# Optimization experiments

Hardware: AMD Instinct MI355X
Metric: run time of the kernel (lower is better)

## Reference

```python
import jax, jax.numpy as jnp
import numpy as np

NUM_HEADS = 32
NUM_KV = 8
HEAD_DIM = 128


def rotate_half(x):
    half = x.shape[-1] // 2
    x1, x2 = x[..., :half], x[..., half:]
    return jnp.concatenate([-x2, x1], axis=-1)


def apply_rope(x, cos, sin):
    # x: [B, H, S, D]; cos/sin: [S, D] broadcast over batch and heads
    return x * cos + rotate_half(x) * sin


def setup_inputs() -> dict:
    key = jax.random.key(0)
    kx, kqkv, kout = jax.random.split(key, 3)
    B, S, H = 2, 2048, 4096
    x = jax.random.normal(kx, (B, S, H), dtype=jnp.float32)
    Wqkv = jax.random.normal(kqkv, (H, NUM_HEADS * HEAD_DIM + 2 * NUM_KV * HEAD_DIM), dtype=jnp.float32) * (H ** -0.5)
    Wout = jax.random.normal(kout, (H, H), dtype=jnp.float32) * (H ** -0.5)
    # realistic RoPE tables (seq, head_dim)
    inv_freq = 1.0 / (10000.0 ** (np.arange(0, HEAD_DIM, 2, dtype=np.float32) / HEAD_DIM))
    freqs = np.outer(np.arange(S, dtype=np.float32), inv_freq)  # [S, D/2]
    emb = np.concatenate([freqs, freqs], axis=-1)  # [S, D]
    cos = jnp.asarray(np.cos(emb), dtype=jnp.float32)
    sin = jnp.asarray(np.sin(emb), dtype=jnp.float32)
    return {"x": x, "cos": cos, "sin": sin, "Wqkv": Wqkv, "Wout": Wout}


def reference(x, cos, sin, Wqkv, Wout):
    B, S, H = x.shape
    nh, nkv, hd = NUM_HEADS, NUM_KV, HEAD_DIM
    qkv = x @ Wqkv  # [B, S, (nh+2*nkv)*hd]
    q, k, v = jnp.split(qkv, [nh * hd, nh * hd + nkv * hd], axis=-1)
    q = q.reshape(B, S, nh, hd).transpose(0, 2, 1, 3)   # [B, nh, S, hd]
    k = k.reshape(B, S, nkv, hd).transpose(0, 2, 1, 3)  # [B, nkv, S, hd]
    v = v.reshape(B, S, nkv, hd).transpose(0, 2, 1, 3)
    q = apply_rope(q, cos, sin)
    k = apply_rope(k, cos, sin)
    group = nh // nkv
    k = jnp.repeat(k, group, axis=1)  # repeat_interleave over head dim
    v = jnp.repeat(v, group, axis=1)
    scale = 1.0 / jnp.sqrt(jnp.asarray(hd, dtype=x.dtype))
    scores = jnp.einsum('bhqd,bhkd->bhqk', q, k) * scale  # [B, nh, S, S]
    causal = jnp.triu(jnp.ones((S, S), dtype=bool), k=1)
    scores = jnp.where(causal, -jnp.inf, scores)
    w = jax.nn.softmax(scores, axis=-1)
    out = jnp.einsum('bhqk,bhkd->bhqd', w, v)  # [B, nh, S, hd]
    out = out.transpose(0, 2, 1, 3).reshape(B, S, nh * hd)
    return out @ Wout
```

## Files before the change

kernel.cpp:

```cpp
#include <hip/hip_runtime.h>

typedef unsigned short u16;
typedef __attribute__((ext_vector_type(8))) short s16x8;
typedef __attribute__((ext_vector_type(4))) short s16x4;
typedef __attribute__((ext_vector_type(4))) float f32x4;

#define DEVI __device__ __forceinline__

DEVI u16 f2b(float f) {
  union { float f; unsigned u; } v; v.f = f;
  unsigned r = v.u + 0x7FFFu + ((v.u >> 16) & 1u);
  return (u16)(r >> 16);
}
DEVI float b2f(u16 h) {
  union { unsigned u; float f; } v; v.u = ((unsigned)h) << 16;
  return v.f;
}

typedef const __attribute__((address_space(1))) void gas_void;
typedef __attribute__((address_space(3))) void las_void;
DEVI void gload16(const void* g, void* l) {
  __builtin_amdgcn_global_load_lds((gas_void*)g, (las_void*)l, 16, 0, 0);
}

__global__ void conv_bf16(const float* __restrict__ in, u16* __restrict__ out, int n8) {
  int i = blockIdx.x * 256 + threadIdx.x;
  if (i >= n8) return;
  const float* p = in + (size_t)i * 8;
  float4 u = *(const float4*)p;
  float4 v = *(const float4*)(p + 4);
  s16x8 o = {(short)f2b(u.x), (short)f2b(u.y), (short)f2b(u.z), (short)f2b(u.w),
             (short)f2b(v.x), (short)f2b(v.y), (short)f2b(v.z), (short)f2b(v.w)};
  *(s16x8*)(out + (size_t)i * 8) = o;
}

__global__ void trans_bf16(const float* __restrict__ W, u16* __restrict__ Wt, int K, int N) {
  __shared__ __attribute__((aligned(16))) u16 tile[64][68];
  const int t = threadIdx.x;
  const int n0 = blockIdx.x * 64, k0 = blockIdx.y * 64;
#pragma unroll
  for (int i = 0; i < 4; ++i) {
    int c = i * 256 + t;
    int r = c >> 4, q = c & 15;
    float4 v = *(const float4*)(W + (size_t)(k0 + r) * N + n0 + q * 4);
    s16x4 o = {(short)f2b(v.x), (short)f2b(v.y), (short)f2b(v.z), (short)f2b(v.w)};
    *(s16x4*)&tile[r][q * 4] = o;
  }
  __syncthreads();
#pragma unroll
  for (int i = 0; i < 2; ++i) {
    int c = i * 256 + t;
    int n_ = c >> 3, ck = (c & 7) * 8;
    s16x8 o;
#pragma unroll
    for (int j = 0; j < 8; ++j) o[j] = (short)tile[ck + j][n_];
    *(s16x8*)(Wt + (size_t)(n0 + n_) * K + k0 + ck) = o;
  }
}

template <typename TC>
__global__ __launch_bounds__(512, 2) void gemm256(const u16* __restrict__ A,
                                                  const u16* __restrict__ Bt,
                                                  TC* __restrict__ C, int M, int N, int K) {
  __shared__ __attribute__((aligned(16))) u16 As[2][2][128 * 64];
  __shared__ __attribute__((aligned(16))) u16 Bs[2][2][128 * 64];
  const int t = threadIdx.x;
  const int nbn = N >> 8;
  const int nwg = (M >> 8) * nbn;
  const int chunk = nwg >> 3;
  const int id = (blockIdx.x & 7) * chunk + (blockIdx.x >> 3);
  const int row0 = (id / nbn) << 8, col0 = (id % nbn) << 8;
  const int w = t >> 6, lane = t & 63, lc = lane & 15, lg = lane >> 4;
  const int wqm = (w >> 2) * 64;
  const int wqn = (w & 3) * 32;
  const int sw7 = lc & 7;

  const f32x4 FZ = {0.f, 0.f, 0.f, 0.f};
  f32x4 acc[4][4][2];
#pragma unroll
  for (int q = 0; q < 4; ++q)
#pragma unroll
    for (int i = 0; i < 4; ++i)
#pragma unroll
      for (int j = 0; j < 2; ++j) acc[q][i][j] = FZ;

  const int s_r0 = t >> 3, s_r1 = (512 + t) >> 3;
  const int s_s = t & 7;

#define STG_A(kt, H, sl)                                                                   \
  {                                                                                        \
    gload16(A + (size_t)(row0 + (H)*128 + s_r0) * K + ((kt) << 6) + ((s_s ^ (s_r0 & 7)) << 3), \
            (u16*)As[sl][H] + t * 8);                                                      \
    gload16(A + (size_t)(row0 + (H)*128 + s_r1) * K + ((kt) << 6) + ((s_s ^ (s_r1 & 7)) << 3), \
            (u16*)As[sl][H] + (512 + t) * 8);                                              \
  }
#define STG_B(kt, H, sl)                                                                   \
  {                                                                                        \
    gload16(Bt + (size_t)(col0 + (H)*128 + s_r0) * K + ((kt) << 6) + ((s_s ^ (s_r0 & 7)) << 3), \
            (u16*)Bs[sl][H] + t * 8);                                                      \
    gload16(Bt + (size_t)(col0 + (H)*128 + s_r1) * K + ((kt) << 6) + ((s_s ^ (s_r1 & 7)) << 3), \
            (u16*)Bs[sl][H] + (512 + t) * 8);                                              \
  }
#define LOAD_A(MH, buf)                                                           \
  _Pragma("unroll") for (int mf = 0; mf < 4; ++mf)                                \
  _Pragma("unroll") for (int ks = 0; ks < 2; ++ks)                                \
    af[mf][ks] = *(const s16x8*)(As[buf][MH] + (wqm + mf * 16 + lc) * 64 +        \
                                 (((ks * 4 + lg) ^ sw7) << 3));
#define LOAD_B(NH, buf, DST)                                                      \
  _Pragma("unroll") for (int nf = 0; nf < 2; ++nf)                                \
  _Pragma("unroll") for (int ks = 0; ks < 2; ++ks)                                \
    DST[nf][ks] = *(const s16x8*)(Bs[buf][NH] + (wqn + nf * 16 + lc) * 64 +       \
                                  (((ks * 4 + lg) ^ sw7) << 3));
#define MFMA_Q(q, BV)                                                             \
  _Pragma("unroll") for (int ks = 0; ks < 2; ++ks)                                \
  _Pragma("unroll") for (int mf = 0; mf < 4; ++mf)                                \
  _Pragma("unroll") for (int nf = 0; nf < 2; ++nf)                                \
    acc[q][mf][nf] = __builtin_amdgcn_mfma_f32_16x16x32_bf16(                     \
        af[mf][ks], BV[nf][ks], acc[q][mf][nf], 0, 0, 0);
#define BAR __builtin_amdgcn_s_barrier()
#define PRIO1 __builtin_amdgcn_s_setprio(1)
#define PRIO0 __builtin_amdgcn_s_setprio(0)
#define WAIT4 asm volatile("s_waitcnt vmcnt(4)" ::: "memory")

  s16x8 af[4][2], bfv0[2][2], bfv1[2][2];
  const int NT = K >> 6, NI = NT >> 1, TM = NT - 1;

  STG_A(0, 0, 0) STG_B(0, 0, 0) STG_B(0, 1, 0) STG_A(0, 1, 0)
  STG_A(1, 0, 1) STG_B(1, 1, 1)
  WAIT4;
  BAR;

  for (int i = 0; i < NI; ++i) {
    const int t1 = 2 * i + 1;
    const int t2 = (2 * i + 2) & TM, t3 = (2 * i + 3) & TM;
    LOAD_A(0, 0) LOAD_B(0, 0, bfv0)
    STG_B(t1, 0, 1)
    BAR; PRIO1; MFMA_Q(0, bfv0) PRIO0; BAR;
    LOAD_B(1, 0, bfv1)
    STG_A(t1, 1, 1)
    BAR; PRIO1; MFMA_Q(1, bfv1) PRIO0; BAR;
    LOAD_A(1, 0)
    STG_A(t2, 0, 0)
    BAR; PRIO1; MFMA_Q(2, bfv1) PRIO0; BAR;
    STG_B(t2, 1, 0)
    BAR; PRIO1; MFMA_Q(3, bfv0) PRIO0;
    WAIT4;
    BAR;
    LOAD_A(0, 1) LOAD_B(0, 1, bfv0)
    STG_B(t2, 0, 0)
    BAR; PRIO1; MFMA_Q(0, bfv0) PRIO0; BAR;
    LOAD_B(1, 1, bfv1)
    STG_A(t2, 1, 0)
    BAR; PRIO1; MFMA_Q(1, bfv1) PRIO0; BAR;
    LOAD_A(1, 1)
    STG_A(t3, 0, 1)
    BAR; PRIO1; MFMA_Q(2, bfv1) PRIO0; BAR;
    STG_B(t3, 1, 1)
    BAR; PRIO1; MFMA_Q(3, bfv0) PRIO0;
    WAIT4;
    BAR;
  }
  asm volatile("s_waitcnt vmcnt(0)" ::: "memory");
  BAR;
#undef STG_A
#undef STG_B
#undef LOAD_A
#undef LOAD_B
#undef MFMA_Q
#undef BAR
#undef PRIO1
#undef PRIO0
#undef WAIT4

  const int qmh[4] = {0, 0, 1, 1}, qnh[4] = {0, 1, 1, 0};
#pragma unroll
  for (int q = 0; q < 4; ++q)
#pragma unroll
    for (int mf = 0; mf < 4; ++mf)
#pragma unroll
      for (int nf = 0; nf < 2; ++nf)
#pragma unroll
        for (int r = 0; r < 4; ++r) {
          const int rg = row0 + qmh[q] * 128 + wqm + mf * 16 + lg * 4 + r;
          const int cg = col0 + qnh[q] * 128 + wqn + nf * 16 + lc;
          if constexpr (sizeof(TC) == 2)
            ((u16*)C)[(size_t)rg * N + cg] = f2b(acc[q][mf][nf][r]);
          else
            ((float*)C)[(size_t)rg * N + cg] = acc[q][mf][nf][r];
        }
}

__global__ void rope_kernel(u16* __restrict__ qkv, const float* __restrict__ cosb,
                            const float* __restrict__ sinb) {
  const int bs = blockIdx.x;
  const int s = bs & 2047;
  u16* row = qkv + (size_t)bs * 6144;
  const float* cr = cosb + s * 128;
  const float* sr = sinb + s * 128;
  for (int p = threadIdx.x; p < 320; p += 256) {
    int head = p >> 3, dc = (p & 7) * 8;
    int ci = head * 128 + dc;
    s16x8 a = *(const s16x8*)&row[ci];
    s16x8 bb = *(const s16x8*)&row[ci + 64];
    float4 c0 = *(const float4*)(cr + dc), c1 = *(const float4*)(cr + dc + 4);
    float4 s0 = *(const float4*)(sr + dc), s1 = *(const float4*)(sr + dc + 4);
    float cv[8] = {c0.x, c0.y, c0.z, c0.w, c1.x, c1.y, c1.z, c1.w};
    float sv[8] = {s0.x, s0.y, s0.z, s0.w, s1.x, s1.y, s1.z, s1.w};
    s16x8 o1, o2;
#pragma unroll
    for (int j = 0; j < 8; ++j) {
      float x1 = b2f((u16)a[j]), x2 = b2f((u16)bb[j]);
      o1[j] = (short)f2b(x1 * cv[j] - x2 * sv[j]);
      o2[j] = (short)f2b(x2 * cv[j] + x1 * sv[j]);
    }
    *(s16x8*)&row[ci] = o1;
    *(s16x8*)&row[ci + 64] = o2;
  }
}

__global__ void vtrans_kernel(const u16* __restrict__ qkv, u16* __restrict__ v_t) {
  __shared__ __attribute__((aligned(16))) u16 tile[64][72];
  const int t = threadIdx.x;
  const int s0 = blockIdx.x * 64;
  const int d0 = blockIdx.y * 64;
  const int bk = blockIdx.z;
  const int b = bk >> 3, kvh = bk & 7;
  const int slot = t & 7, r0 = t >> 3;
#pragma unroll
  for (int i = 0; i < 2; ++i) {
    int s_ = r0 + 32 * i;
    *(s16x8*)&tile[s_][slot * 8] =
        *(const s16x8*)(qkv + (size_t)(b * 2048 + s0 + s_) * 6144 + 5120 + kvh * 128 + d0 + slot * 8);
  }
  __syncthreads();
#pragma unroll
  for (int i = 0; i < 2; ++i) {
    int d_ = r0 + 32 * i;
    s16x8 v;
#pragma unroll
    for (int j = 0; j < 8; ++j) v[j] = (short)tile[slot * 8 + j][d_];
    *(s16x8*)(v_t + ((size_t)bk * 128 + d0 + d_) * 2048 + s0 + slot * 8) = v;
  }
}

__global__ void __launch_bounds__(256, 2) attn_kernel(const u16* __restrict__ qkv,
                                                      const u16* __restrict__ v_t,
                                                      u16* __restrict__ attn) {
  __shared__ __attribute__((aligned(16))) u16 Ks[64][136];
  __shared__ __attribute__((aligned(16))) u16 Vs[128][72];
  __shared__ __attribute__((aligned(16))) u16 Ps[4][32][72];
  const int t = threadIdx.x;
  const int f = blockIdx.x;
  const int xcd = f & 7, ix = f >> 3;
  const int g = (xcd << 1) | (ix >> 6);
  const int r_ = ix & 63;
  const int b = g >> 3, kvh = g & 7;
  const int qt = 15 - (r_ >> 2);
  const int h = kvh * 4 + (r_ & 3);
  const int q0 = qt * 128;
  const int w = t >> 6, lane = t & 63, lc = lane & 15, lg = lane >> 4;
  const int qw = q0 + w * 32;

  const u16* qbase = qkv + (size_t)(b * 2048) * 6144 + h * 128;
  const u16* kbase = qkv + (size_t)(b * 2048) * 6144 + 4096 + kvh * 128;
  const u16* vbase = v_t + (size_t)(b * 8 + kvh) * 128 * 2048;

  s16x8 qf[2][4];
#pragma unroll
  for (int mf = 0; mf < 2; ++mf)
#pragma unroll
    for (int ks = 0; ks < 4; ++ks)
      qf[mf][ks] = *(const s16x8*)(qbase + (size_t)(qw + mf * 16 + lc) * 6144 + ks * 32 + lg * 8);

  const f32x4 FZ = {0.f, 0.f, 0.f, 0.f};
  f32x4 o_acc[2][8];
  float m_run[2][4], l_run[2][4];
#pragma unroll
  for (int mf = 0; mf < 2; ++mf) {
#pragma unroll
    for (int nf = 0; nf < 8; ++nf) o_acc[mf][nf] = FZ;
#pragma unroll
    for (int r = 0; r < 4; ++r) { m_run[mf][r] = -3e38f; l_run[mf][r] = 0.f; }
  }
  const float scale2 = 0.08838834764831845f * 1.44269504088896340736f;

  const int ntiles = q0 / 64 + 2;
  s16x8 kr[4], vr[4];
#pragma unroll
  for (int i = 0; i < 4; ++i) {
    int c = i * 256 + t;
    kr[i] = *(const s16x8*)(kbase + (size_t)(c >> 4) * 6144 + (c & 15) * 8);
    vr[i] = *(const s16x8*)(vbase + (size_t)(c >> 3) * 2048 + (c & 7) * 8);
  }

  for (int kt = 0; kt < ntiles; ++kt) {
    const int k0 = kt * 64;
    __syncthreads();
#pragma unroll
    for (int i = 0; i < 4; ++i) {
      int c = i * 256 + t;
      *(s16x8*)&Ks[c >> 4][(c & 15) * 8] = kr[i];
      *(s16x8*)&Vs[c >> 3][(c & 7) * 8] = vr[i];
    }
    __syncthreads();
    if (kt + 1 < ntiles) {
      int k1 = k0 + 64;
#pragma unroll
      for (int i = 0; i < 4; ++i) {
        int c = i * 256 + t;
        kr[i] = *(const s16x8*)(kbase + (size_t)(k1 + (c >> 4)) * 6144 + (c & 15) * 8);
        vr[i] = *(const s16x8*)(vbase + (size_t)(c >> 3) * 2048 + k1 + (c & 7) * 8);
      }
    }
    if (k0 > qw + 31) continue;

    f32x4 sacc[2][4];
#pragma unroll
    for (int mf = 0; mf < 2; ++mf)
#pragma unroll
      for (int nf = 0; nf < 4; ++nf) sacc[mf][nf] = FZ;
#pragma unroll
    for (int ks = 0; ks < 4; ++ks) {
      s16x8 kf[4];
#pragma unroll
      for (int nf = 0; nf < 4; ++nf)
        kf[nf] = *(const s16x8*)&Ks[nf * 16 + lc][ks * 32 + lg * 8];
#pragma unroll
      for (int mf = 0; mf < 2; ++mf)
#pragma unroll
        for (int nf = 0; nf < 4; ++nf)
          sacc[mf][nf] = __builtin_amdgcn_mfma_f32_16x16x32_bf16(qf[mf][ks], kf[nf], sacc[mf][nf], 0, 0, 0);
    }

#pragma unroll
    for (int mf = 0; mf < 2; ++mf) {
      float pm[4] = {-3e38f, -3e38f, -3e38f, -3e38f};
      const bool dm = (k0 + 63 > qw + mf * 16);
      if (dm) {
#pragma unroll
        for (int nf = 0; nf < 4; ++nf) {
          int kv = k0 + nf * 16 + lc;
#pragma unroll
          for (int r = 0; r < 4; ++r) {
            int qg = qw + mf * 16 + lg * 4 + r;
            float sv = sacc[mf][nf][r] * scale2;
            sv = (kv <= qg) ? sv : -3e38f;
            sacc[mf][nf][r] = sv;
            pm[r] = fmaxf(pm[r], sv);
          }
        }
      } else {
#pragma unroll
        for (int nf = 0; nf < 4; ++nf)
#pragma unroll
          for (int r = 0; r < 4; ++r) {
            float sv = sacc[mf][nf][r] * scale2;
            sacc[mf][nf][r] = sv;
            pm[r] = fmaxf(pm[r], sv);
          }
      }
#pragma unroll
      for (int r = 0; r < 4; ++r) {
        pm[r] = fmaxf(pm[r], __shfl_xor(pm[r], 1));
        pm[r] = fmaxf(pm[r], __shfl_xor(pm[r], 2));
        pm[r] = fmaxf(pm[r], __shfl_xor(pm[r], 4));
        pm[r] = fmaxf(pm[r], __shfl_xor(pm[r], 8));
      }
      bool any = false;
      float mnew[4];
#pragma unroll
      for (int r = 0; r < 4; ++r) {
        mnew[r] = fmaxf(m_run[mf][r], pm[r]);
        any |= (mnew[r] > m_run[mf][r]);
      }
      if (__any(any)) {
#pragma unroll
        for (int r = 0; r < 4; ++r) {
          float fsc = exp2f(m_run[mf][r] - mnew[r]);
          m_run[mf][r] = mnew[r];
          l_run[mf][r] *= fsc;
#pragma unroll
          for (int nf = 0; nf < 8; ++nf) o_acc[mf][nf][r] *= fsc;
        }
      }
      float psum[4] = {0.f, 0.f, 0.f, 0.f};
#pragma unroll
      for (int nf = 0; nf < 4; ++nf)
#pragma unroll
        for (int r = 0; r < 4; ++r) {
          float p = exp2f(sacc[mf][nf][r] - m_run[mf][r]);
          psum[r] += p;
          Ps[w][mf * 16 + lg * 4 + r][nf * 16 + lc] = f2b(p);
        }
#pragma unroll
      for (int r = 0; r < 4; ++r) {
        float ps = psum[r];
        ps += __shfl_xor(ps, 1);
        ps += __shfl_xor(ps, 2);
        ps += __shfl_xor(ps, 4);
        ps += __shfl_xor(ps, 8);
        l_run[mf][r] += ps;
      }
    }
#pragma unroll
    for (int ks = 0; ks < 2; ++ks) {
      s16x8 pf[2];
#pragma unroll
      for (int mf = 0; mf < 2; ++mf)
        pf[mf] = *(const s16x8*)&Ps[w][mf * 16 + lc][ks * 32 + lg * 8];
#pragma unroll
      for (int nf = 0; nf < 8; ++nf) {
        s16x8 vf = *(const s16x8*)&Vs[nf * 16 + lc][ks * 32 + lg * 8];
#pragma unroll
        for (int mf = 0; mf < 2; ++mf)
          o_acc[mf][nf] = __builtin_amdgcn_mfma_f32_16x16x32_bf16(pf[mf], vf, o_acc[mf][nf], 0, 0, 0);
      }
    }
  }

#pragma unroll
  for (int mf = 0; mf < 2; ++mf)
#pragma unroll
    for (int r = 0; r < 4; ++r) {
      float inv = 1.0f / l_run[mf][r];
      int qg = qw + mf * 16 + lg * 4 + r;
#pragma unroll
      for (int nf = 0; nf < 8; ++nf)
        attn[(size_t)(b * 2048 + qg) * 4096 + h * 128 + nf * 16 + lc] =
            f2b(o_acc[mf][nf][r] * inv);
    }
}

extern "C" void kernel_launch(void* const* d_in, const int* in_sizes, int n_in,
                              void* d_out, int out_size, void* d_ws, size_t ws_size,
                              hipStream_t stream) {
  (void)in_sizes; (void)n_in; (void)out_size; (void)ws_size;
  const float* x = (const float*)d_in[0];
  const float* cosb = (const float*)d_in[1];
  const float* sinb = (const float*)d_in[2];
  const float* Wqkv = (const float*)d_in[3];
  const float* Wout = (const float*)d_in[4];
  float* out = (float*)d_out;
  char* ws = (char*)d_ws;

  u16* buf0 = (u16*)ws;
  u16* buf1 = (u16*)(ws + 50331648);
  u16* regc = (u16*)(ws + 100663296);

  conv_bf16<<<8192, 256, 0, stream>>>(x, regc, 2097152);
  trans_bf16<<<dim3(96, 64), 256, 0, stream>>>(Wqkv, buf0, 4096, 6144);
  gemm256<u16><<<384, 512, 0, stream>>>(regc, buf0, buf1, 4096, 6144, 4096);
  rope_kernel<<<4096, 256, 0, stream>>>(buf1, cosb, sinb);
  vtrans_kernel<<<dim3(32, 2, 16), 256, 0, stream>>>(buf1, regc);
  attn_kernel<<<1024, 256, 0, stream>>>(buf1, regc, buf0);
  trans_bf16<<<dim3(64, 64), 256, 0, stream>>>(Wout, regc, 4096, 4096);
  gemm256<float><<<256, 512, 0, stream>>>(buf0, regc, out, 4096, 4096, 4096);
}
```

Measured before the change: 580.1 us.

## Deepen GEMM prefetch pipeline with per-k-tile loop and vmcnt(6) wait

Restructures the GEMM main loop from a two-tile unrolled body into a single per-k-tile loop. Each iteration stages the remaining half of tile k+1 plus three quarters of tile k+2, and the loop waits with vmcnt(6) instead of vmcnt(4). This keeps more global-to-LDS loads in flight so memory latency hides better behind the MFMA quarters. In exchange, the buffer reuse timing becomes more intricate, which risks LDS hazards if a stage overwrites data that is still being read.

```diff
diff --git a/kernel.cpp b/kernel.cpp
--- a/kernel.cpp
+++ b/kernel.cpp
@@ -120,44 +120,31 @@
 #define BAR __builtin_amdgcn_s_barrier()
 #define PRIO1 __builtin_amdgcn_s_setprio(1)
 #define PRIO0 __builtin_amdgcn_s_setprio(0)
-#define WAIT4 asm volatile("s_waitcnt vmcnt(4)" ::: "memory")
+#define WAIT6 asm volatile("s_waitcnt vmcnt(6)" ::: "memory")
 
   s16x8 af[4][2], bfv0[2][2], bfv1[2][2];
-  const int NT = K >> 6, NI = NT >> 1, TM = NT - 1;
+  const int NT = K >> 6, TM = NT - 1;
 
   STG_A(0, 0, 0) STG_B(0, 0, 0) STG_B(0, 1, 0) STG_A(0, 1, 0)
-  STG_A(1, 0, 1) STG_B(1, 1, 1)
-  WAIT4;
+  STG_A(1, 0, 1) STG_B(1, 0, 1) STG_B(1, 1, 1)
+  WAIT6;
   BAR;
 
-  for (int i = 0; i < NI; ++i) {
-    const int t1 = 2 * i + 1;
-    const int t2 = (2 * i + 2) & TM, t3 = (2 * i + 3) & TM;
-    LOAD_A(0, 0) LOAD_B(0, 0, bfv0)
-    STG_B(t1, 0, 1)
+  for (int kt = 0; kt < NT; ++kt) {
+    const int buf = kt & 1, nb = buf ^ 1;
+    const int tp1 = (kt + 1) & TM, tp2 = (kt + 2) & TM;
+    LOAD_A(0, buf) LOAD_B(0, buf, bfv0)
+    STG_A(tp1, 1, nb)
     BAR; PRIO1; MFMA_Q(0, bfv0) PRIO0; BAR;
-    LOAD_B(1, 0, bfv1)
-    STG_A(t1, 1, 1)
+    LOAD_B(1, buf, bfv1)
+    STG_A(tp2, 0, buf)
     BAR; PRIO1; MFMA_Q(1, bfv1) PRIO0; BAR;
-    LOAD_A(1, 0)
-    STG_A(t2, 0, 0)
+    LOAD_A(1, buf)
+    STG_B(tp2, 0, buf)
     BAR; PRIO1; MFMA_Q(2, bfv1) PRIO0; BAR;
-    STG_B(t2, 1, 0)
+    STG_B(tp2, 1, buf)
     BAR; PRIO1; MFMA_Q(3, bfv0) PRIO0;
-    WAIT4;
-    BAR;
-    LOAD_A(0, 1) LOAD_B(0, 1, bfv0)
-    STG_B(t2, 0, 0)
-    BAR; PRIO1; MFMA_Q(0, bfv0) PRIO0; BAR;
-    LOAD_B(1, 1, bfv1)
-    STG_A(t2, 1, 0)
-    BAR; PRIO1; MFMA_Q(1, bfv1) PRIO0; BAR;
-    LOAD_A(1, 1)
-    STG_A(t3, 0, 1)
-    BAR; PRIO1; MFMA_Q(2, bfv1) PRIO0; BAR;
-    STG_B(t3, 1, 1)
-    BAR; PRIO1; MFMA_Q(3, bfv0) PRIO0;
-    WAIT4;
+    WAIT6;
     BAR;
   }
   asm volatile("s_waitcnt vmcnt(0)" ::: "memory");
@@ -170,7 +157,7 @@
 #undef BAR
 #undef PRIO1
 #undef PRIO0
-#undef WAIT4
+#undef WAIT6
 
   const int qmh[4] = {0, 0, 1, 1}, qnh[4] = {0, 1, 1, 0};
 #pragma unroll
```

Result: faster. 567.8 us (-2.1%).
